# Performance work log

Hardware: AMD Instinct MI355X
Metric: run time of the kernel (lower is better)

## Reference

```python
import jax, jax.numpy as jnp
import numpy as np

N_NODES = 50000
N_EDGES = 800000
IN_FEAT = 128
HID = 128
OUT = 10
N_GRAPHS = 128
BN_EPS = 1e-5


def setup_inputs() -> dict:
    key = jax.random.key(0)
    ks = jax.random.split(key, 16)
    inp = {
        "n_feat": jax.random.normal(ks[0], (N_NODES, IN_FEAT), dtype=jnp.float32),
        "src": jax.random.randint(ks[1], (N_EDGES,), 0, N_NODES),
        "dst": jax.random.randint(ks[2], (N_EDGES,), 0, N_NODES),
        "graph_ids": jnp.sort(jax.random.randint(ks[3], (N_NODES,), 0, N_GRAPHS)),
        # GraphConv weights (DGL layout: weight [in, out], bias [out])
        "W1": jax.random.normal(ks[4], (IN_FEAT, HID), dtype=jnp.float32) / np.sqrt(IN_FEAT),
        "b1": jnp.zeros((HID,), dtype=jnp.float32),
        "W2": jax.random.normal(ks[5], (HID, HID), dtype=jnp.float32) / np.sqrt(HID),
        "b2": jnp.zeros((HID,), dtype=jnp.float32),
        # BatchNorm1d affine params
        "gamma": jnp.ones((HID,), dtype=jnp.float32),
        "beta": jnp.zeros((HID,), dtype=jnp.float32),
        # MLP head
        "fc1_w": jax.random.normal(ks[6], (HID, HID), dtype=jnp.float32) / np.sqrt(HID),
        "fc1_b": jnp.zeros((HID,), dtype=jnp.float32),
        "fc2_w": jax.random.normal(ks[7], (HID, OUT), dtype=jnp.float32) / np.sqrt(HID),
        "fc2_b": jnp.zeros((OUT,), dtype=jnp.float32),
    }
    return inp


def _graph_conv(x, W, b, src, dst, inv_sqrt_out, inv_sqrt_in):
    # DGL GraphConv, norm='both': h = D_in^{-1/2} A D_out^{-1/2} x W + b
    h = x * inv_sqrt_out[:, None]          # [N, d_in]
    h = h @ W                              # [N, d_out] (project before gather: fewer bytes moved)
    agg = jax.ops.segment_sum(h[src], dst, num_segments=N_NODES)  # gather + scatter-add
    return agg * inv_sqrt_in[:, None] + b


def reference(n_feat, src, dst, graph_ids, W1, b1, W2, b2, gamma, beta,
              fc1_w, fc1_b, fc2_w, fc2_b):
    ones_e = jnp.ones((N_EDGES,), dtype=jnp.float32)
    deg_out = jnp.clip(jax.ops.segment_sum(ones_e, src, num_segments=N_NODES), 1.0)
    deg_in = jnp.clip(jax.ops.segment_sum(ones_e, dst, num_segments=N_NODES), 1.0)
    inv_sqrt_out = jax.lax.rsqrt(deg_out)
    inv_sqrt_in = jax.lax.rsqrt(deg_in)

    x = jax.nn.relu(_graph_conv(n_feat, W1, b1, src, dst, inv_sqrt_out, inv_sqrt_in))
    # dropout is identity in eval mode
    x = jax.nn.relu(_graph_conv(x, W2, b2, src, dst, inv_sqrt_out, inv_sqrt_in))

    # SumPooling over graphs
    embedding = jax.ops.segment_sum(x, graph_ids, num_segments=N_GRAPHS)  # [B, HID]

    # BatchNorm1d (training-mode batch stats, biased variance like torch)
    mu = jnp.mean(embedding, axis=0)
    var = jnp.mean(jnp.square(embedding - mu), axis=0)
    h = gamma * (embedding - mu) * jax.lax.rsqrt(var + BN_EPS) + beta

    h = jax.nn.relu(h @ fc1_w + fc1_b)
    logits = h @ fc2_w + fc2_b
    return embedding, jax.nn.log_softmax(logits, axis=-1)
```

## Files before the change

kernel.cpp:

```cpp
#include <hip/hip_runtime.h>
#include <hip/hip_bf16.h>
#include <math.h>

#define N_NODES 50000
#define N_EDGES 800000
#define HID 128
#define N_GRAPHS 128
#define OUTC 10
#define BN_EPS 1e-5f

#define SCAN_B 256
#define N_SCAN_BLOCKS ((N_NODES + SCAN_B - 1) / SCAN_B)

#define POOL_CHUNK 32
#define N_POOL_BLOCKS ((N_NODES + POOL_CHUNK - 1) / POOL_CHUNK)

#define HB 80
#define HWORDS (N_NODES / 2)

#define EPAD 8
#define E_SRC_CAP (N_EDGES + N_NODES * EPAD)

#define LDA 136

typedef short short8 __attribute__((ext_vector_type(8)));
typedef float floatx4 __attribute__((ext_vector_type(4)));

template <typename T, typename F>
__device__ inline T bitcast(F f) {
    union { F a; T b; } u;
    u.a = f;
    return u.b;
}

__global__ __launch_bounds__(1024) void hist_part_kernel(const int* __restrict__ src,
                                                         const int* __restrict__ dst,
                                                         unsigned int* __restrict__ part) {
    __shared__ unsigned int h[HWORDS];
    for (int i = threadIdx.x; i < HWORDS; i += 1024) h[i] = 0;
    __syncthreads();
    int half = (blockIdx.x >= HB) ? 1 : 0;
    const int* __restrict__ idx = half ? dst : src;
    int b = blockIdx.x - half * HB;
    for (int e = b * 1024 + threadIdx.x; e < N_EDGES; e += HB * 1024) {
        int v = idx[e];
        atomicAdd(&h[v >> 1], 1u << ((v & 1) << 4));
    }
    __syncthreads();
    unsigned int* __restrict__ out = part + (size_t)blockIdx.x * HWORDS;
    for (int i = threadIdx.x; i < HWORDS; i += 1024) out[i] = h[i];
}

__global__ void hist_reduce_kernel(unsigned int* __restrict__ part,
                                   int* __restrict__ cnt_in,
                                   float* __restrict__ inv_out, float* __restrict__ inv_in) {
    int w = blockIdx.x * blockDim.x + threadIdx.x;
    if (w >= HWORDS) return;
    unsigned int s = 0, d = 0;
    for (int b = 0; b < HB; b++) {
        s += part[(size_t)b * HWORDS + w];
        unsigned int c = part[(size_t)(b + HB) * HWORDS + w];
        part[(size_t)(b + HB) * HWORDS + w] = d;
        d += c;
    }
    int i0 = w * 2, i1 = i0 + 1;
    int so0 = (int)(s & 0xFFFFu), so1 = (int)(s >> 16);
    int di0 = (int)(d & 0xFFFFu), di1 = (int)(d >> 16);
    cnt_in[i0] = di0;
    cnt_in[i1] = di1;
    inv_out[i0] = rsqrtf(fmaxf((float)so0, 1.0f));
    inv_out[i1] = rsqrtf(fmaxf((float)so1, 1.0f));
    inv_in[i0] = rsqrtf(fmaxf((float)di0, 1.0f));
    inv_in[i1] = rsqrtf(fmaxf((float)di1, 1.0f));
}

__global__ void scan_sum_kernel(const int* __restrict__ cnt, int* __restrict__ bsum) {
    int i = blockIdx.x * SCAN_B + threadIdx.x;
    int v = (i < N_NODES) ? ((cnt[i] + EPAD - 1) & ~(EPAD - 1)) : 0;
#pragma unroll
    for (int o = 32; o > 0; o >>= 1) v += __shfl_down(v, o);
    __shared__ int ws[4];
    int wave = threadIdx.x >> 6, lane = threadIdx.x & 63;
    if (lane == 0) ws[wave] = v;
    __syncthreads();
    if (threadIdx.x == 0) bsum[blockIdx.x] = ws[0] + ws[1] + ws[2] + ws[3];
}

__global__ void scan_bsum_kernel(const int* __restrict__ bsum, int* __restrict__ boff) {
    __shared__ int part[SCAN_B];
    int t = threadIdx.x;
    int v = (t < N_SCAN_BLOCKS) ? bsum[t] : 0;
    part[t] = v;
    __syncthreads();
    for (int off = 1; off < SCAN_B; off <<= 1) {
        int u = (t >= off) ? part[t - off] : 0;
        __syncthreads();
        part[t] += u;
        __syncthreads();
    }
    boff[t] = part[t] - v;
}

__global__ void scan_write_kernel(const int* __restrict__ cnt, const int* __restrict__ boff,
                                  int* __restrict__ row_ptr) {
    __shared__ int part[SCAN_B];
    int t = threadIdx.x;
    int i = blockIdx.x * SCAN_B + t;
    int v = (i < N_NODES) ? ((cnt[i] + EPAD - 1) & ~(EPAD - 1)) : 0;
    part[t] = v;
    __syncthreads();
    for (int off = 1; off < SCAN_B; off <<= 1) {
        int u = (t >= off) ? part[t - off] : 0;
        __syncthreads();
        part[t] += u;
        __syncthreads();
    }
    if (i < N_NODES) {
        int ex = part[t] - v + boff[blockIdx.x];
        row_ptr[i] = ex;
        if (i == N_NODES - 1) row_ptr[N_NODES] = ex + v;
    }
}

__global__ __launch_bounds__(1024) void csr_fill_kernel(const int* __restrict__ src,
                                                        const int* __restrict__ dst,
                                                        const unsigned int* __restrict__ part,
                                                        const int* __restrict__ row_ptr,
                                                        int* __restrict__ edge_src) {
    __shared__ unsigned int loc[HWORDS];
    int b = blockIdx.x;
    const unsigned int* __restrict__ off = part + (size_t)(b + HB) * HWORDS;
    for (int i = threadIdx.x; i < HWORDS; i += 1024) loc[i] = off[i];
    __syncthreads();
    for (int e = b * 1024 + threadIdx.x; e < N_EDGES; e += HB * 1024) {
        int d = dst[e];
        unsigned int old = atomicAdd(&loc[d >> 1], 1u << ((d & 1) << 4));
        int local = (d & 1) ? (int)(old >> 16) : (int)(old & 0xFFFFu);
        edge_src[row_ptr[d] + local] = src[e];
    }
}

__global__ void fill_pad_kernel(const int* __restrict__ row_ptr, const int* __restrict__ cnt,
                                int* __restrict__ edge_src) {
    int n = blockIdx.x * blockDim.x + threadIdx.x;
    if (n < N_NODES) {
        int p = row_ptr[n] + cnt[n];
        int e = row_ptr[n + 1];
        for (; p < e; p++) edge_src[p] = N_NODES;
    }
}

__global__ __launch_bounds__(64) void wpack_kernel(const float* __restrict__ W1,
                                                   const float* __restrict__ W2,
                                                   unsigned short* __restrict__ Wp) {
    int b = blockIdx.x;
    int wi = b >> 5;
    const float* __restrict__ W = wi ? W2 : W1;
    int t = b & 31;
    int kc = t >> 3, nt = t & 7;
    int lane = threadIdx.x;
    int n = lane & 15, quad = lane >> 4;
    unsigned short v[8];
#pragma unroll
    for (int j = 0; j < 8; j++) {
        int k = kc * 32 + quad * 8 + j;
        v[j] = __hip_bfloat16_raw(__float2bfloat16(W[k * HID + nt * 16 + n])).x;
    }
    unsigned short* out = Wp + ((size_t)wi * 32 * 64 + (size_t)(kc * 8 + nt) * 64 + lane) * 8;
    *(uint4*)out = *(uint4*)v;
}

__global__ __launch_bounds__(256) void matmul_kernel(const float* __restrict__ X,
                                                     const float* __restrict__ scale,
                                                     const unsigned short* __restrict__ Wp,
                                                     __hip_bfloat16* __restrict__ Y) {
    __shared__ unsigned short xs[64 * LDA];
    int tid = threadIdx.x;
    int row0 = blockIdx.x * 64;

    for (int j = 0; j < 8; j++) {
        int idx4 = j * 256 + tid;
        int r = idx4 >> 5;
        int col = (idx4 & 31) * 4;
        int rg = row0 + r;
        float4 v = make_float4(0.f, 0.f, 0.f, 0.f);
        if (rg < N_NODES) {
            v = *(const float4*)&X[(size_t)rg * HID + col];
            float sc = scale[rg];
            v.x *= sc; v.y *= sc; v.z *= sc; v.w *= sc;
        }
        unsigned short o[4];
        o[0] = __hip_bfloat16_raw(__float2bfloat16(v.x)).x;
        o[1] = __hip_bfloat16_raw(__float2bfloat16(v.y)).x;
        o[2] = __hip_bfloat16_raw(__float2bfloat16(v.z)).x;
        o[3] = __hip_bfloat16_raw(__float2bfloat16(v.w)).x;
        *(ushort4*)&xs[r * LDA + col] = *(ushort4*)o;
    }
    __syncthreads();

    int wave = tid >> 6, lane = tid & 63;
    int m = lane & 15, quad = lane >> 4;
    int rowl = wave * 16;

    short8 a[4];
#pragma unroll
    for (int kc = 0; kc < 4; kc++)
        a[kc] = bitcast<short8>(*(const uint4*)&xs[(rowl + m) * LDA + kc * 32 + quad * 8]);

    floatx4 acc[8];
#pragma unroll
    for (int nt = 0; nt < 8; nt++) acc[nt] = (floatx4){0.f, 0.f, 0.f, 0.f};

#pragma unroll
    for (int nt = 0; nt < 8; nt++) {
#pragma unroll
        for (int kc = 0; kc < 4; kc++) {
            short8 bfr = bitcast<short8>(
                *(const uint4*)&Wp[((size_t)(kc * 8 + nt) * 64 + lane) * 8]);
            acc[nt] = __builtin_amdgcn_mfma_f32_16x16x32_bf16(a[kc], bfr, acc[nt], 0, 0, 0);
        }
    }

#pragma unroll
    for (int nt = 0; nt < 8; nt++) {
#pragma unroll
        for (int i = 0; i < 4; i++) {
            int rg = row0 + rowl + quad * 4 + i;
            if (rg < N_NODES + 1) {
                Y[(size_t)rg * HID + nt * 16 + m] = __float2bfloat16(acc[nt][i]);
            }
        }
    }
}

__global__ __launch_bounds__(256) void agg_kernel(const __hip_bfloat16* __restrict__ Y,
                                                  const int* __restrict__ edge_src,
                                                  const int* __restrict__ row_ptr,
                                                  const float* __restrict__ inv_in,
                                                  const float* __restrict__ bias,
                                                  float* __restrict__ Xout) {
    const uint4* __restrict__ Yq = (const uint4*)Y;
    int wave = threadIdx.x >> 6;
    int lane = threadIdx.x & 63;
    int n = blockIdx.x * 4 + wave;
    if (n >= N_NODES) return;
    int beg = row_ptr[n], end = row_ptr[n + 1];
    int esub = lane >> 4;
    int f16  = lane & 15;
    float acc[8] = {};
    for (int base = beg; base < end; base += 64) {
        int mm = min(64, end - base);
        int idx = (lane < mm) ? edge_src[base + lane] : N_NODES;
        for (int j = 0; j < mm; j += 8) {
            int s0 = __shfl(idx, j + esub);
            int s1 = __shfl(idx, j + 4 + esub);
            uint4 u0 = Yq[s0 * (HID / 8) + f16];
            uint4 u1 = Yq[s1 * (HID / 8) + f16];
            acc[0] += __uint_as_float(u0.x << 16); acc[1] += __uint_as_float(u0.x & 0xFFFF0000u);
            acc[2] += __uint_as_float(u0.y << 16); acc[3] += __uint_as_float(u0.y & 0xFFFF0000u);
            acc[4] += __uint_as_float(u0.z << 16); acc[5] += __uint_as_float(u0.z & 0xFFFF0000u);
            acc[6] += __uint_as_float(u0.w << 16); acc[7] += __uint_as_float(u0.w & 0xFFFF0000u);
            acc[0] += __uint_as_float(u1.x << 16); acc[1] += __uint_as_float(u1.x & 0xFFFF0000u);
            acc[2] += __uint_as_float(u1.y << 16); acc[3] += __uint_as_float(u1.y & 0xFFFF0000u);
            acc[4] += __uint_as_float(u1.z << 16); acc[5] += __uint_as_float(u1.z & 0xFFFF0000u);
            acc[6] += __uint_as_float(u1.w << 16); acc[7] += __uint_as_float(u1.w & 0xFFFF0000u);
        }
    }
#pragma unroll
    for (int i = 0; i < 8; i++) {
        acc[i] += __shfl_xor(acc[i], 16);
        acc[i] += __shfl_xor(acc[i], 32);
    }
    if (lane < 16) {
        float si = inv_in[n];
        int f0 = f16 * 8;
        float4 b0 = *(const float4*)&bias[f0];
        float4 b1 = *(const float4*)&bias[f0 + 4];
        float4 o0, o1;
        o0.x = fmaxf(acc[0] * si + b0.x, 0.f);
        o0.y = fmaxf(acc[1] * si + b0.y, 0.f);
        o0.z = fmaxf(acc[2] * si + b0.z, 0.f);
        o0.w = fmaxf(acc[3] * si + b0.w, 0.f);
        o1.x = fmaxf(acc[4] * si + b1.x, 0.f);
        o1.y = fmaxf(acc[5] * si + b1.y, 0.f);
        o1.z = fmaxf(acc[6] * si + b1.z, 0.f);
        o1.w = fmaxf(acc[7] * si + b1.w, 0.f);
        *(float4*)&Xout[(size_t)n * HID + f0] = o0;
        *(float4*)&Xout[(size_t)n * HID + f0 + 4] = o1;
    }
}

__global__ __launch_bounds__(64) void pool_kernel(const float* __restrict__ X,
                                                  const int* __restrict__ gid,
                                                  float* __restrict__ emb) {
    int lane = threadIdx.x;
    int n0 = blockIdx.x * POOL_CHUNK;
    int n1 = min(n0 + POOL_CHUNK, N_NODES);
    if (n0 >= N_NODES) return;
    int g_cur = gid[n0];
    float ax = 0.f, ay = 0.f;
    for (int n = n0; n < n1; n++) {
        int g = gid[n];
        if (g != g_cur) {
            atomicAdd(&emb[g_cur * HID + lane * 2], ax);
            atomicAdd(&emb[g_cur * HID + lane * 2 + 1], ay);
            ax = 0.f; ay = 0.f;
            g_cur = g;
        }
        float2 v = *(const float2*)&X[(size_t)n * HID + lane * 2];
        ax += v.x;
        ay += v.y;
    }
    atomicAdd(&emb[g_cur * HID + lane * 2], ax);
    atomicAdd(&emb[g_cur * HID + lane * 2 + 1], ay);
}

__global__ void bnstats_kernel(const float* __restrict__ emb, const float* __restrict__ gamma,
                               const float* __restrict__ beta, float* __restrict__ scale,
                               float* __restrict__ shift) {
    int f = threadIdx.x;
    float s = 0.f;
    for (int r = 0; r < N_GRAPHS; r++) s += emb[r * HID + f];
    float mu = s * (1.f / N_GRAPHS);
    float v = 0.f;
    for (int r = 0; r < N_GRAPHS; r++) {
        float d = emb[r * HID + f] - mu;
        v += d * d;
    }
    v *= (1.f / N_GRAPHS);
    float sc = gamma[f] * rsqrtf(v + BN_EPS);
    scale[f] = sc;
    shift[f] = beta[f] - mu * sc;
}

__global__ void fc1_kernel(const float* __restrict__ emb, const float* __restrict__ scale,
                           const float* __restrict__ shift, const float* __restrict__ W,
                           const float* __restrict__ b, float* __restrict__ H) {
    __shared__ float xr[HID];
    int r = blockIdx.x, c = threadIdx.x;
    xr[c] = emb[r * HID + c] * scale[c] + shift[c];
    __syncthreads();
    float acc = b[c];
    for (int k = 0; k < HID; k++) acc += xr[k] * W[k * HID + c];
    H[r * HID + c] = fmaxf(acc, 0.f);
}

__global__ void head_kernel(const float* __restrict__ H, const float* __restrict__ W,
                            const float* __restrict__ b, float* __restrict__ out) {
    __shared__ float hr[HID];
    __shared__ float logits[OUTC];
    __shared__ float mstat[2];
    int r = blockIdx.x, t = threadIdx.x;
    hr[t] = H[r * HID + t];
    hr[t + 64] = H[r * HID + t + 64];
    __syncthreads();
    if (t < OUTC) {
        float acc = b[t];
        for (int k = 0; k < HID; k++) acc += hr[k] * W[k * OUTC + t];
        logits[t] = acc;
    }
    __syncthreads();
    if (t == 0) {
        float m = logits[0];
        for (int o = 1; o < OUTC; o++) m = fmaxf(m, logits[o]);
        float sum = 0.f;
        for (int o = 0; o < OUTC; o++) sum += expf(logits[o] - m);
        mstat[0] = m;
        mstat[1] = logf(sum);
    }
    __syncthreads();
    if (t < OUTC) out[r * OUTC + t] = logits[t] - mstat[0] - mstat[1];
}

extern "C" void kernel_launch(void* const* d_in, const int* in_sizes, int n_in,
                              void* d_out, int out_size, void* d_ws, size_t ws_size,
                              hipStream_t stream) {
    const float* n_feat = (const float*)d_in[0];
    const int*   src    = (const int*)d_in[1];
    const int*   dst    = (const int*)d_in[2];
    const int*   gid    = (const int*)d_in[3];
    const float* W1     = (const float*)d_in[4];
    const float* b1     = (const float*)d_in[5];
    const float* W2     = (const float*)d_in[6];
    const float* b2     = (const float*)d_in[7];
    const float* gamma  = (const float*)d_in[8];
    const float* beta   = (const float*)d_in[9];
    const float* fc1_w  = (const float*)d_in[10];
    const float* fc1_b  = (const float*)d_in[11];
    const float* fc2_w  = (const float*)d_in[12];
    const float* fc2_b  = (const float*)d_in[13];

    char* wsb = (char*)d_ws;
    size_t off = 0;
    auto alloc = [&](size_t bytes) -> void* {
        void* p = wsb + off;
        off += (bytes + 255) & ~(size_t)255;
        return p;
    };
    int*   cnt_in  = (int*)alloc((size_t)N_NODES * 4);
    int*   row_ptr = (int*)alloc((size_t)(N_NODES + 1) * 4);
    int*   e_src   = (int*)alloc((size_t)E_SRC_CAP * 4);
    float* inv_out = (float*)alloc((size_t)N_NODES * 4);
    float* inv_in  = (float*)alloc((size_t)N_NODES * 4);
    void*  ybuf    = alloc((size_t)2 * HB * HWORDS * 4);
    float* X       = (float*)alloc((size_t)N_NODES * HID * 4);
    unsigned short* Wp = (unsigned short*)alloc((size_t)2 * 32 * 64 * 8 * 2);
    float* scale   = (float*)alloc(HID * 4);
    float* shift   = (float*)alloc(HID * 4);
    float* H       = (float*)alloc((size_t)N_GRAPHS * HID * 4);
    int*   bsum    = (int*)alloc((size_t)SCAN_B * 4);
    int*   boff    = (int*)alloc((size_t)SCAN_B * 4);

    unsigned int*   part = (unsigned int*)ybuf;
    __hip_bfloat16* Y    = (__hip_bfloat16*)ybuf;

    float* emb_out = (float*)d_out;
    float* lsm_out = emb_out + N_GRAPHS * HID;

    hipMemsetAsync(emb_out, 0, (size_t)N_GRAPHS * HID * 4, stream);

    hist_part_kernel<<<2 * HB, 1024, 0, stream>>>(src, dst, part);
    wpack_kernel<<<64, 64, 0, stream>>>(W1, W2, Wp);
    hist_reduce_kernel<<<(HWORDS + 255) / 256, 256, 0, stream>>>(part, cnt_in, inv_out, inv_in);
    scan_sum_kernel<<<N_SCAN_BLOCKS, SCAN_B, 0, stream>>>(cnt_in, bsum);
    scan_bsum_kernel<<<1, SCAN_B, 0, stream>>>(bsum, boff);
    scan_write_kernel<<<N_SCAN_BLOCKS, SCAN_B, 0, stream>>>(cnt_in, boff, row_ptr);
    csr_fill_kernel<<<HB, 1024, 0, stream>>>(src, dst, part, row_ptr, e_src);
    fill_pad_kernel<<<(N_NODES + 255) / 256, 256, 0, stream>>>(row_ptr, cnt_in, e_src);

    matmul_kernel<<<(N_NODES + 64) / 64, 256, 0, stream>>>(n_feat, inv_out, Wp, Y);
    agg_kernel<<<(N_NODES + 3) / 4, 256, 0, stream>>>(Y, e_src, row_ptr, inv_in, b1, X);
    matmul_kernel<<<(N_NODES + 64) / 64, 256, 0, stream>>>(X, inv_out, Wp + (size_t)32 * 64 * 8, Y);
    agg_kernel<<<(N_NODES + 3) / 4, 256, 0, stream>>>(Y, e_src, row_ptr, inv_in, b2, X);

    pool_kernel<<<N_POOL_BLOCKS, 64, 0, stream>>>(X, gid, emb_out);
    bnstats_kernel<<<1, HID, 0, stream>>>(emb_out, gamma, beta, scale, shift);
    fc1_kernel<<<N_GRAPHS, HID, 0, stream>>>(emb_out, scale, shift, fc1_w, fc1_b, H);
    head_kernel<<<N_GRAPHS, 64, 0, stream>>>(H, fc2_w, fc2_b, lsm_out);
}
```

Before: 261.3 us.

## Fuse small preprocessing and head kernels to cut launch count

Folds the weight packing into an extra block of the histogram kernel and computes the scan block sums inside hist_reduce. Block sizes are aligned so each block covers 256 nodes, matching the scan blocks. It also writes edge padding inside scan_write and merges the BN-stats, fc1 and head kernels into one kernel. The aim is to remove five kernel launches and their serialization gaps on the stream. In exchange, every head block redundantly recomputes the BatchNorm statistics over the full embedding.

Measured after the change: 255.4 us (median of 2 runs). 1.02x faster.

```diff
diff --git a/kernel.cpp b/kernel.cpp
--- a/kernel.cpp
+++ b/kernel.cpp
@@ -17,6 +17,8 @@
 
 #define HB 80
 #define HWORDS (N_NODES / 2)
+#define HR_B 128
+#define HR_BLOCKS ((HWORDS + HR_B - 1) / HR_B)
 
 #define EPAD 8
 #define E_SRC_CAP (N_EDGES + N_NODES * EPAD)
@@ -35,7 +37,28 @@
 
 __global__ __launch_bounds__(1024) void hist_part_kernel(const int* __restrict__ src,
                                                          const int* __restrict__ dst,
-                                                         unsigned int* __restrict__ part) {
+                                                         unsigned int* __restrict__ part,
+                                                         const float* __restrict__ W1,
+                                                         const float* __restrict__ W2,
+                                                         unsigned short* __restrict__ Wp) {
+    if (blockIdx.x == 2 * HB) {
+        for (int q = threadIdx.x; q < 4096; q += 1024) {
+            int wi = q >> 11;
+            const float* __restrict__ W = wi ? W2 : W1;
+            int t2 = q & 2047;
+            int tile = t2 >> 6, lane = t2 & 63;
+            int kc = tile >> 3, nt = tile & 7;
+            int n = lane & 15, quad = lane >> 4;
+            unsigned short v[8];
+#pragma unroll
+            for (int j = 0; j < 8; j++) {
+                int k = kc * 32 + quad * 8 + j;
+                v[j] = __hip_bfloat16_raw(__float2bfloat16(W[k * HID + nt * 16 + n])).x;
+            }
+            *(uint4*)&Wp[(size_t)q * 8] = *(uint4*)v;
+        }
+        return;
+    }
     __shared__ unsigned int h[HWORDS];
     for (int i = threadIdx.x; i < HWORDS; i += 1024) h[i] = 0;
     __syncthreads();
@@ -51,39 +74,40 @@
     for (int i = threadIdx.x; i < HWORDS; i += 1024) out[i] = h[i];
 }
 
-__global__ void hist_reduce_kernel(unsigned int* __restrict__ part,
-                                   int* __restrict__ cnt_in,
-                                   float* __restrict__ inv_out, float* __restrict__ inv_in) {
-    int w = blockIdx.x * blockDim.x + threadIdx.x;
-    if (w >= HWORDS) return;
-    unsigned int s = 0, d = 0;
-    for (int b = 0; b < HB; b++) {
-        s += part[(size_t)b * HWORDS + w];
-        unsigned int c = part[(size_t)(b + HB) * HWORDS + w];
-        part[(size_t)(b + HB) * HWORDS + w] = d;
-        d += c;
-    }
-    int i0 = w * 2, i1 = i0 + 1;
-    int so0 = (int)(s & 0xFFFFu), so1 = (int)(s >> 16);
-    int di0 = (int)(d & 0xFFFFu), di1 = (int)(d >> 16);
-    cnt_in[i0] = di0;
-    cnt_in[i1] = di1;
-    inv_out[i0] = rsqrtf(fmaxf((float)so0, 1.0f));
-    inv_out[i1] = rsqrtf(fmaxf((float)so1, 1.0f));
-    inv_in[i0] = rsqrtf(fmaxf((float)di0, 1.0f));
-    inv_in[i1] = rsqrtf(fmaxf((float)di1, 1.0f));
-}
-
-__global__ void scan_sum_kernel(const int* __restrict__ cnt, int* __restrict__ bsum) {
-    int i = blockIdx.x * SCAN_B + threadIdx.x;
-    int v = (i < N_NODES) ? ((cnt[i] + EPAD - 1) & ~(EPAD - 1)) : 0;
-#pragma unroll
-    for (int o = 32; o > 0; o >>= 1) v += __shfl_down(v, o);
-    __shared__ int ws[4];
-    int wave = threadIdx.x >> 6, lane = threadIdx.x & 63;
-    if (lane == 0) ws[wave] = v;
-    __syncthreads();
-    if (threadIdx.x == 0) bsum[blockIdx.x] = ws[0] + ws[1] + ws[2] + ws[3];
+__global__ __launch_bounds__(HR_B) void hist_reduce_kernel(unsigned int* __restrict__ part,
+                                                           int* __restrict__ cnt_in,
+                                                           float* __restrict__ inv_out,
+                                                           float* __restrict__ inv_in,
+                                                           int* __restrict__ bsum) {
+    int w = blockIdx.x * HR_B + threadIdx.x;
+    int padsum = 0;
+    if (w < HWORDS) {
+        unsigned int s = 0, d = 0;
+        for (int b = 0; b < HB; b++) {
+            s += part[(size_t)b * HWORDS + w];
+            unsigned int c = part[(size_t)(b + HB) * HWORDS + w];
+            part[(size_t)(b + HB) * HWORDS + w] = d;
+            d += c;
+        }
+        int i0 = w * 2, i1 = i0 + 1;
+        int so0 = (int)(s & 0xFFFFu), so1 = (int)(s >> 16);
+        int di0 = (int)(d & 0xFFFFu), di1 = (int)(d >> 16);
+        cnt_in[i0] = di0;
+        cnt_in[i1] = di1;
+        inv_out[i0] = rsqrtf(fmaxf((float)so0, 1.0f));
+        inv_out[i1] = rsqrtf(fmaxf((float)so1, 1.0f));
+        inv_in[i0] = rsqrtf(fmaxf((float)di0, 1.0f));
+        inv_in[i1] = rsqrtf(fmaxf((float)di1, 1.0f));
+        padsum = ((di0 + EPAD - 1) & ~(EPAD - 1)) + ((di1 + EPAD - 1) & ~(EPAD - 1));
+    }
+    __shared__ int red[HR_B];
+    red[threadIdx.x] = padsum;
+    __syncthreads();
+    for (int o = HR_B / 2; o > 0; o >>= 1) {
+        if (threadIdx.x < o) red[threadIdx.x] += red[threadIdx.x + o];
+        __syncthreads();
+    }
+    if (threadIdx.x == 0) bsum[blockIdx.x] = red[0];
 }
 
 __global__ void scan_bsum_kernel(const int* __restrict__ bsum, int* __restrict__ boff) {
@@ -102,11 +126,12 @@
 }
 
 __global__ void scan_write_kernel(const int* __restrict__ cnt, const int* __restrict__ boff,
-                                  int* __restrict__ row_ptr) {
+                                  int* __restrict__ row_ptr, int* __restrict__ edge_src) {
     __shared__ int part[SCAN_B];
     int t = threadIdx.x;
     int i = blockIdx.x * SCAN_B + t;
-    int v = (i < N_NODES) ? ((cnt[i] + EPAD - 1) & ~(EPAD - 1)) : 0;
+    int raw = (i < N_NODES) ? cnt[i] : 0;
+    int v = (raw + EPAD - 1) & ~(EPAD - 1);
     part[t] = v;
     __syncthreads();
     for (int off = 1; off < SCAN_B; off <<= 1) {
@@ -118,6 +143,7 @@
     if (i < N_NODES) {
         int ex = part[t] - v + boff[blockIdx.x];
         row_ptr[i] = ex;
+        for (int p = ex + raw; p < ex + v; p++) edge_src[p] = N_NODES;
         if (i == N_NODES - 1) row_ptr[N_NODES] = ex + v;
     }
 }
@@ -138,36 +164,6 @@
         int local = (d & 1) ? (int)(old >> 16) : (int)(old & 0xFFFFu);
         edge_src[row_ptr[d] + local] = src[e];
     }
-}
-
-__global__ void fill_pad_kernel(const int* __restrict__ row_ptr, const int* __restrict__ cnt,
-                                int* __restrict__ edge_src) {
-    int n = blockIdx.x * blockDim.x + threadIdx.x;
-    if (n < N_NODES) {
-        int p = row_ptr[n] + cnt[n];
-        int e = row_ptr[n + 1];
-        for (; p < e; p++) edge_src[p] = N_NODES;
-    }
-}
-
-__global__ __launch_bounds__(64) void wpack_kernel(const float* __restrict__ W1,
-                                                   const float* __restrict__ W2,
-                                                   unsigned short* __restrict__ Wp) {
-    int b = blockIdx.x;
-    int wi = b >> 5;
-    const float* __restrict__ W = wi ? W2 : W1;
-    int t = b & 31;
-    int kc = t >> 3, nt = t & 7;
-    int lane = threadIdx.x;
-    int n = lane & 15, quad = lane >> 4;
-    unsigned short v[8];
-#pragma unroll
-    for (int j = 0; j < 8; j++) {
-        int k = kc * 32 + quad * 8 + j;
-        v[j] = __hip_bfloat16_raw(__float2bfloat16(W[k * HID + nt * 16 + n])).x;
-    }
-    unsigned short* out = Wp + ((size_t)wi * 32 * 64 + (size_t)(kc * 8 + nt) * 64 + lane) * 8;
-    *(uint4*)out = *(uint4*)v;
 }
 
 __global__ __launch_bounds__(256) void matmul_kernel(const float* __restrict__ X,
@@ -315,52 +311,45 @@
     atomicAdd(&emb[g_cur * HID + lane * 2 + 1], ay);
 }
 
-__global__ void bnstats_kernel(const float* __restrict__ emb, const float* __restrict__ gamma,
-                               const float* __restrict__ beta, float* __restrict__ scale,
-                               float* __restrict__ shift) {
-    int f = threadIdx.x;
+__global__ __launch_bounds__(128) void head_fused_kernel(const float* __restrict__ emb,
+                                                         const float* __restrict__ gamma,
+                                                         const float* __restrict__ beta,
+                                                         const float* __restrict__ fc1_w,
+                                                         const float* __restrict__ fc1_b,
+                                                         const float* __restrict__ fc2_w,
+                                                         const float* __restrict__ fc2_b,
+                                                         float* __restrict__ out) {
+    int r = blockIdx.x, f = threadIdx.x;
     float s = 0.f;
-    for (int r = 0; r < N_GRAPHS; r++) s += emb[r * HID + f];
+    for (int row = 0; row < N_GRAPHS; row++) s += emb[row * HID + f];
     float mu = s * (1.f / N_GRAPHS);
     float v = 0.f;
-    for (int r = 0; r < N_GRAPHS; r++) {
-        float d = emb[r * HID + f] - mu;
+    for (int row = 0; row < N_GRAPHS; row++) {
+        float d = emb[row * HID + f] - mu;
         v += d * d;
     }
     v *= (1.f / N_GRAPHS);
     float sc = gamma[f] * rsqrtf(v + BN_EPS);
-    scale[f] = sc;
-    shift[f] = beta[f] - mu * sc;
-}
-
-__global__ void fc1_kernel(const float* __restrict__ emb, const float* __restrict__ scale,
-                           const float* __restrict__ shift, const float* __restrict__ W,
-                           const float* __restrict__ b, float* __restrict__ H) {
+    float sh = beta[f] - mu * sc;
+
     __shared__ float xr[HID];
-    int r = blockIdx.x, c = threadIdx.x;
-    xr[c] = emb[r * HID + c] * scale[c] + shift[c];
-    __syncthreads();
-    float acc = b[c];
-    for (int k = 0; k < HID; k++) acc += xr[k] * W[k * HID + c];
-    H[r * HID + c] = fmaxf(acc, 0.f);
-}
-
-__global__ void head_kernel(const float* __restrict__ H, const float* __restrict__ W,
-                            const float* __restrict__ b, float* __restrict__ out) {
+    xr[f] = emb[r * HID + f] * sc + sh;
+    __syncthreads();
+    float acc = fc1_b[f];
+    for (int k = 0; k < HID; k++) acc += xr[k] * fc1_w[k * HID + f];
     __shared__ float hr[HID];
+    hr[f] = fmaxf(acc, 0.f);
+    __syncthreads();
+
     __shared__ float logits[OUTC];
     __shared__ float mstat[2];
-    int r = blockIdx.x, t = threadIdx.x;
-    hr[t] = H[r * HID + t];
-    hr[t + 64] = H[r * HID + t + 64];
-    __syncthreads();
-    if (t < OUTC) {
-        float acc = b[t];
-        for (int k = 0; k < HID; k++) acc += hr[k] * W[k * OUTC + t];
-        logits[t] = acc;
-    }
-    __syncthreads();
-    if (t == 0) {
+    if (f < OUTC) {
+        float a = fc2_b[f];
+        for (int k = 0; k < HID; k++) a += hr[k] * fc2_w[k * OUTC + f];
+        logits[f] = a;
+    }
+    __syncthreads();
+    if (f == 0) {
         float m = logits[0];
         for (int o = 1; o < OUTC; o++) m = fmaxf(m, logits[o]);
         float sum = 0.f;
@@ -369,7 +358,7 @@
         mstat[1] = logf(sum);
     }
     __syncthreads();
-    if (t < OUTC) out[r * OUTC + t] = logits[t] - mstat[0] - mstat[1];
+    if (f < OUTC) out[r * OUTC + f] = logits[f] - mstat[0] - mstat[1];
 }
 
 extern "C" void kernel_launch(void* const* d_in, const int* in_sizes, int n_in,
@@ -405,9 +394,6 @@
     void*  ybuf    = alloc((size_t)2 * HB * HWORDS * 4);
     float* X       = (float*)alloc((size_t)N_NODES * HID * 4);
     unsigned short* Wp = (unsigned short*)alloc((size_t)2 * 32 * 64 * 8 * 2);
-    float* scale   = (float*)alloc(HID * 4);
-    float* shift   = (float*)alloc(HID * 4);
-    float* H       = (float*)alloc((size_t)N_GRAPHS * HID * 4);
     int*   bsum    = (int*)alloc((size_t)SCAN_B * 4);
     int*   boff    = (int*)alloc((size_t)SCAN_B * 4);
 
@@ -419,14 +405,11 @@
 
     hipMemsetAsync(emb_out, 0, (size_t)N_GRAPHS * HID * 4, stream);
 
-    hist_part_kernel<<<2 * HB, 1024, 0, stream>>>(src, dst, part);
-    wpack_kernel<<<64, 64, 0, stream>>>(W1, W2, Wp);
-    hist_reduce_kernel<<<(HWORDS + 255) / 256, 256, 0, stream>>>(part, cnt_in, inv_out, inv_in);
-    scan_sum_kernel<<<N_SCAN_BLOCKS, SCAN_B, 0, stream>>>(cnt_in, bsum);
+    hist_part_kernel<<<2 * HB + 1, 1024, 0, stream>>>(src, dst, part, W1, W2, Wp);
+    hist_reduce_kernel<<<HR_BLOCKS, HR_B, 0, stream>>>(part, cnt_in, inv_out, inv_in, bsum);
     scan_bsum_kernel<<<1, SCAN_B, 0, stream>>>(bsum, boff);
-    scan_write_kernel<<<N_SCAN_BLOCKS, SCAN_B, 0, stream>>>(cnt_in, boff, row_ptr);
+    scan_write_kernel<<<N_SCAN_BLOCKS, SCAN_B, 0, stream>>>(cnt_in, boff, row_ptr, e_src);
     csr_fill_kernel<<<HB, 1024, 0, stream>>>(src, dst, part, row_ptr, e_src);
-    fill_pad_kernel<<<(N_NODES + 255) / 256, 256, 0, stream>>>(row_ptr, cnt_in, e_src);
 
     matmul_kernel<<<(N_NODES + 64) / 64, 256, 0, stream>>>(n_feat, inv_out, Wp, Y);
     agg_kernel<<<(N_NODES + 3) / 4, 256, 0, stream>>>(Y, e_src, row_ptr, inv_in, b1, X);
@@ -434,7 +417,6 @@
     agg_kernel<<<(N_NODES + 3) / 4, 256, 0, stream>>>(Y, e_src, row_ptr, inv_in, b2, X);
 
     pool_kernel<<<N_POOL_BLOCKS, 64, 0, stream>>>(X, gid, emb_out);
-    bnstats_kernel<<<1, HID, 0, stream>>>(emb_out, gamma, beta, scale, shift);
-    fc1_kernel<<<N_GRAPHS, HID, 0, stream>>>(emb_out, scale, shift, fc1_w, fc1_b, H);
-    head_kernel<<<N_GRAPHS, 64, 0, stream>>>(H, fc2_w, fc2_b, lsm_out);
-}
+    head_fused_kernel<<<N_GRAPHS, HID, 0, stream>>>(emb_out, gamma, beta, fc1_w, fc1_b,
+                                                    fc2_w, fc2_b, lsm_out);
+}
```
